# Optimization experiments

Hardware: AMD Instinct MI355X
Metric: run time of the kernel (lower is better)

The kernel has to match this reference:

```python
import jax, jax.numpy as jnp
import numpy as np

H = 1024          # hidden_size
E = 2 * H         # expansion e
S_DIM = 128       # shared q/k dim s
B, S = 4, 2048


def setup_inputs() -> dict:
    key = jax.random.key(0)
    ks = jax.random.split(key, 6)
    inputs = jax.random.normal(ks[0], (B, S, H), dtype=jnp.float32)
    W_uv = jax.random.normal(ks[1], (H, 2 * E + S_DIM), dtype=jnp.float32) * (1.0 / np.sqrt(H))
    b_uv = jnp.zeros((2 * E + S_DIM,), dtype=jnp.float32)
    gamma = jax.random.normal(ks[2], (2, S_DIM), dtype=jnp.float32) * 0.02
    beta = jnp.zeros((2, S_DIM), dtype=jnp.float32)
    W_out = jax.random.normal(ks[3], (E, H), dtype=jnp.float32) * (1.0 / np.sqrt(E))
    b_out = jnp.zeros((H,), dtype=jnp.float32)
    return {"inputs": inputs, "W_uv": W_uv, "b_uv": b_uv,
            "gamma": gamma, "beta": beta, "W_out": W_out, "b_out": b_out}


def reference(inputs, W_uv, b_uv, gamma, beta, W_out, b_out):
    seq_len = inputs.shape[1]
    # uv projection + SiLU
    uvb = jax.nn.silu(jnp.einsum('bsh,hf->bsf', inputs, W_uv) + b_uv)
    u = uvb[..., :E]                       # [B,S,E]
    v = uvb[..., E:2 * E]                  # [B,S,E]
    base = uvb[..., 2 * E:]                # [B,S,s]
    # per-head affine: [B,S,1,s]*[2,s] + [2,s] -> [B,S,2,s]
    qk = base[..., None, :] * gamma + beta
    q, k = qk[..., 0, :], qk[..., 1, :]    # [B,S,s] each
    scores = jnp.einsum('bns,bms->bnm', q, k) / seq_len   # [B,S,S]
    sq = jnp.square(jax.nn.relu(scores))
    attn_v = jnp.einsum('bnm,bme->bne', sq, v)            # [B,S,E]
    return jnp.einsum('bne,eh->bnh', u * attn_v, W_out) + b_out
```

## Files before the change

### kernel.cpp

```cpp
#include <hip/hip_runtime.h>
#include <stdint.h>


#define H_DIM  1024
#define E_DIM  2048
#define SD     128
#define B_SZ   4
#define S_LEN  2048
#define M_TOT  (B_SZ * S_LEN)
#define F_DIM  (2 * E_DIM + SD)

typedef _Float16 f16;
typedef __attribute__((ext_vector_type(4))) _Float16 f16x4;
typedef __attribute__((ext_vector_type(8))) _Float16 f16x8;
typedef __attribute__((ext_vector_type(4))) float f32x4;

__device__ __forceinline__ float silu_f(float x) { return x / (1.f + __expf(-x)); }

__device__ __forceinline__ void gload16(const void* g, void* l) {
  __builtin_amdgcn_global_load_lds(
      (const __attribute__((address_space(1))) void*)(uintptr_t)g,
      (__attribute__((address_space(3))) void*)(uint32_t)(uintptr_t)l,
      16, 0, 0);
}

__global__ __launch_bounds__(256) void cast_f16_k(const float* __restrict__ src,
                                                  f16* __restrict__ dst, long n) {
  long i = ((long)blockIdx.x * 256 + threadIdx.x) * 4;
  if (i < n) {
    float4 v = *(const float4*)(src + i);
    f16x4 h; h[0] = (f16)v.x; h[1] = (f16)v.y; h[2] = (f16)v.z; h[3] = (f16)v.w;
    *(f16x4*)(dst + i) = h;
  }
}

__global__ __launch_bounds__(256) void transpose_cast_k(const float* __restrict__ src,
                                                        f16* __restrict__ dst, int R, int C) {
  __shared__ float tile[32][33];
  int c0 = blockIdx.x * 32, r0 = blockIdx.y * 32;
  int tx = threadIdx.x & 31, ty = threadIdx.x >> 5;
  for (int i = ty; i < 32; i += 8) tile[i][tx] = src[(long)(r0 + i) * C + c0 + tx];
  __syncthreads();
  for (int i = ty; i < 32; i += 8) dst[(long)(c0 + i) * R + r0 + tx] = (f16)tile[tx][i];
}

template <int MODE>
__global__ __launch_bounds__(256) void mfma_gemm(
    const f16* __restrict__ Ag, const f16* __restrict__ Bg,
    float* __restrict__ F0, f16* __restrict__ H0, const f16* __restrict__ H1,
    f16* __restrict__ H2, f16* __restrict__ H3,
    const float* __restrict__ C0, const float* __restrict__ C1,
    const float* __restrict__ C2)
{
  constexpr int K   = (MODE == 1) ? SD : (MODE == 0 || MODE == 4) ? H_DIM : 2048;
  constexpr int LDA = K, LDB = K;

  __shared__ f16 As[128][32];
  __shared__ f16 Bs[128][32];

  const int t    = threadIdx.x;
  const int w    = t >> 6;
  const int lane = t & 63;
  const int l16  = lane & 15;
  const int quad = lane >> 4;
  const int wy   = w >> 1, wx = w & 1;
  const int m0   = blockIdx.y * 128;
  const int n0   = blockIdx.x * 128;
  const long z   = blockIdx.z;

  const f16* A = Ag + (MODE == 1 ? z * (long)S_LEN * SD
                     : MODE == 2 ? z * (long)S_LEN * S_LEN : 0);
  const f16* B = Bg + (MODE == 1 ? z * (long)S_LEN * SD
                     : MODE == 2 ? z * (long)E_DIM * S_LEN : 0);

  const int srow = lane >> 2;
  const int scol = (lane & 3) * 8;

  f32x4 acc[4][4] = {};

  for (int k0 = 0; k0 < K; k0 += 32) {
    const f16* gA = A + (long)(m0 + (w << 5) + srow) * LDA + k0 + scol;
    const f16* gB = B + (long)(n0 + (w << 5) + srow) * LDB + k0 + scol;
    gload16(gA,                  &As[(w << 5)][0]);
    gload16(gA + (long)16 * LDA, &As[(w << 5) + 16][0]);
    gload16(gB,                  &Bs[(w << 5)][0]);
    gload16(gB + (long)16 * LDB, &Bs[(w << 5) + 16][0]);
    __syncthreads();

    f16x8 av[4], bv[4];
#pragma unroll
    for (int i = 0; i < 4; i++)
      av[i] = *(const f16x8*)&As[(wy << 6) + (i << 4) + l16][quad << 3];
#pragma unroll
    for (int j = 0; j < 4; j++)
      bv[j] = *(const f16x8*)&Bs[(wx << 6) + (j << 4) + l16][quad << 3];
#pragma unroll
    for (int i = 0; i < 4; i++)
#pragma unroll
      for (int j = 0; j < 4; j++)
        acc[i][j] = __builtin_amdgcn_mfma_f32_16x16x32_f16(av[i], bv[j], acc[i][j], 0, 0, 0);
    __syncthreads();
  }

  const int rbase = m0 + (wy << 6) + (quad << 2);
  const int cbase = n0 + (wx << 6) + l16;

  if (MODE == 0) {
    if (n0 < E_DIM) {
#pragma unroll
      for (int i = 0; i < 4; i++)
#pragma unroll
        for (int j = 0; j < 4; j++) {
          int gc = cbase + (j << 4);
          float bias = C0[gc];
#pragma unroll
          for (int r = 0; r < 4; r++) {
            int gr = rbase + (i << 4) + r;
            H0[(long)gr * E_DIM + gc] = (f16)silu_f(acc[i][j][r] + bias);
          }
        }
    } else {
#pragma unroll
      for (int i = 0; i < 4; i++) {
        int gr0 = rbase + (i << 4);
        int b   = gr0 >> 11;
        int s0  = gr0 & (S_LEN - 1);
#pragma unroll
        for (int j = 0; j < 4; j++) {
          int gc = cbase + (j << 4);
          float bias = C0[gc];
          f16x4 pk;
#pragma unroll
          for (int r = 0; r < 4; r++) pk[r] = (f16)silu_f(acc[i][j][r] + bias);
          *(f16x4*)&H1[((long)b * E_DIM + (gc - E_DIM)) * S_LEN + s0] = pk;
        }
      }
    }
  } else if (MODE == 4) {
#pragma unroll
    for (int i = 0; i < 4; i++)
#pragma unroll
      for (int j = 0; j < 4; j++) {
        int jj = cbase + (j << 4);
        float bias = C0[jj];
        float g0 = C1[jj], g1 = C1[SD + jj];
        float be0 = C2[jj], be1 = C2[SD + jj];
#pragma unroll
        for (int r = 0; r < 4; r++) {
          int gr = rbase + (i << 4) + r;
          float s = silu_f(acc[i][j][r] + bias);
          H2[(long)gr * SD + jj] = (f16)(s * g0 + be0);
          H3[(long)gr * SD + jj] = (f16)(s * g1 + be1);
        }
      }
  } else if (MODE == 1) {
#pragma unroll
    for (int i = 0; i < 4; i++)
#pragma unroll
      for (int j = 0; j < 4; j++) {
        int gc = cbase + (j << 4);
#pragma unroll
        for (int r = 0; r < 4; r++) {
          int gr = rbase + (i << 4) + r;
          float tv = fmaxf(acc[i][j][r], 0.f) * 64.f;
          H0[z * (long)S_LEN * S_LEN + (long)gr * S_LEN + gc] = (f16)(tv * tv);
        }
      }
  } else if (MODE == 2) {
    const long rowoff = z * S_LEN;
#pragma unroll
    for (int i = 0; i < 4; i++)
#pragma unroll
      for (int j = 0; j < 4; j++) {
        int gc = cbase + (j << 4);
#pragma unroll
        for (int r = 0; r < 4; r++) {
          int gr = rbase + (i << 4) + r;
          long idx = (rowoff + gr) * (long)E_DIM + gc;
          H0[idx] = (f16)((float)H1[idx] * acc[i][j][r]);
        }
      }
  } else {
#pragma unroll
    for (int i = 0; i < 4; i++)
#pragma unroll
      for (int j = 0; j < 4; j++) {
        int gc = cbase + (j << 4);
        float bias = C0[gc];
#pragma unroll
        for (int r = 0; r < 4; r++) {
          int gr = rbase + (i << 4) + r;
          F0[(long)gr * H_DIM + gc] = acc[i][j][r] * (1.0f / 17179869184.0f) + bias;
        }
      }
  }
}

extern "C" void kernel_launch(void* const* d_in, const int* in_sizes, int n_in,
                              void* d_out, int out_size, void* d_ws, size_t ws_size,
                              hipStream_t stream) {
  const float* X     = (const float*)d_in[0];
  const float* W_uv  = (const float*)d_in[1];
  const float* b_uv  = (const float*)d_in[2];
  const float* gamma = (const float*)d_in[3];
  const float* beta  = (const float*)d_in[4];
  const float* W_out = (const float*)d_in[5];
  const float* b_out = (const float*)d_in[6];
  float* out = (float*)d_out;

  char* wp = (char*)d_ws;
  f16* Xh   = (f16*)wp; wp += (long)M_TOT * H_DIM * 2;
  f16* Wuvt = (f16*)wp; wp += (long)F_DIM * H_DIM * 2;
  f16* Wt   = (f16*)wp; wp += (long)H_DIM * E_DIM * 2;
  f16* u    = (f16*)wp; wp += (long)M_TOT * E_DIM * 2;
  f16* vt   = (f16*)wp; wp += (long)M_TOT * E_DIM * 2;
  f16* qh   = (f16*)wp; wp += (long)M_TOT * SD * 2;
  f16* kh   = (f16*)wp; wp += (long)M_TOT * SD * 2;
  f16* sq   = (f16*)wp; wp += (long)B_SZ * S_LEN * S_LEN * 2;
  f16* p    = (f16*)wp; wp += (long)M_TOT * E_DIM * 2;

  cast_f16_k<<<(M_TOT * H_DIM) / (256 * 4), 256, 0, stream>>>(X, Xh, (long)M_TOT * H_DIM);
  transpose_cast_k<<<dim3(F_DIM / 32, H_DIM / 32), 256, 0, stream>>>(W_uv, Wuvt, H_DIM, F_DIM);
  transpose_cast_k<<<dim3(H_DIM / 32, E_DIM / 32), 256, 0, stream>>>(W_out, Wt, E_DIM, H_DIM);

  mfma_gemm<0><<<dim3(2 * E_DIM / 128, M_TOT / 128, 1), 256, 0, stream>>>(
      Xh, Wuvt, nullptr, u, vt, nullptr, nullptr, b_uv, nullptr, nullptr);

  mfma_gemm<4><<<dim3(1, M_TOT / 128, 1), 256, 0, stream>>>(
      Xh, Wuvt + (long)2 * E_DIM * H_DIM, nullptr, nullptr, nullptr, qh, kh,
      b_uv + 2 * E_DIM, gamma, beta);

  mfma_gemm<1><<<dim3(S_LEN / 128, S_LEN / 128, B_SZ), 256, 0, stream>>>(
      qh, kh, nullptr, sq, nullptr, nullptr, nullptr, nullptr, nullptr, nullptr);

  mfma_gemm<2><<<dim3(E_DIM / 128, S_LEN / 128, B_SZ), 256, 0, stream>>>(
      sq, vt, nullptr, p, u, nullptr, nullptr, nullptr, nullptr, nullptr);

  mfma_gemm<3><<<dim3(H_DIM / 128, M_TOT / 128, 1), 256, 0, stream>>>(
      p, Wt, out, nullptr, nullptr, nullptr, nullptr, b_out, nullptr, nullptr);
}
```

Measured before the change: 404.7 us.

## Switch GEMM core to 32x32x16 MFMA with 64-wide K steps

Each wave now uses 2x2 tiles of the 32x32x16 f16 MFMA instead of 4x4 tiles of 16x16x32, and every K iteration loads 64 elements into two LDS halves. This halves the number of barrier pairs and cuts LDS fragment reads per MFMA, aiming for higher matrix-core throughput. Epilogue index math is rewritten for the 32x32 output layout. LDS use doubles, and there is still no overlap between loads and compute, and possible LDS bank conflicts.

Result: no change. 411.2 us (+1.6%).

```diff
diff --git a/kernel.cpp b/kernel.cpp
--- a/kernel.cpp
+++ b/kernel.cpp
@@ -13,7 +13,7 @@
 typedef _Float16 f16;
 typedef __attribute__((ext_vector_type(4))) _Float16 f16x4;
 typedef __attribute__((ext_vector_type(8))) _Float16 f16x8;
-typedef __attribute__((ext_vector_type(4))) float f32x4;
+typedef __attribute__((ext_vector_type(16))) float f32x16;
 
 __device__ __forceinline__ float silu_f(float x) { return x / (1.f + __expf(-x)); }
 
@@ -55,14 +55,14 @@
   constexpr int K   = (MODE == 1) ? SD : (MODE == 0 || MODE == 4) ? H_DIM : 2048;
   constexpr int LDA = K, LDB = K;
 
-  __shared__ f16 As[128][32];
-  __shared__ f16 Bs[128][32];
+  __shared__ f16 As[2][128][32];
+  __shared__ f16 Bs[2][128][32];
 
   const int t    = threadIdx.x;
   const int w    = t >> 6;
   const int lane = t & 63;
-  const int l16  = lane & 15;
-  const int quad = lane >> 4;
+  const int lo5  = lane & 31;
+  const int hi   = lane >> 5;
   const int wy   = w >> 1, wx = w & 1;
   const int m0   = blockIdx.y * 128;
   const int n0   = blockIdx.x * 128;
@@ -76,122 +76,142 @@
   const int srow = lane >> 2;
   const int scol = (lane & 3) * 8;
 
-  f32x4 acc[4][4] = {};
-
-  for (int k0 = 0; k0 < K; k0 += 32) {
-    const f16* gA = A + (long)(m0 + (w << 5) + srow) * LDA + k0 + scol;
-    const f16* gB = B + (long)(n0 + (w << 5) + srow) * LDB + k0 + scol;
-    gload16(gA,                  &As[(w << 5)][0]);
-    gload16(gA + (long)16 * LDA, &As[(w << 5) + 16][0]);
-    gload16(gB,                  &Bs[(w << 5)][0]);
-    gload16(gB + (long)16 * LDB, &Bs[(w << 5) + 16][0]);
+  f32x16 acc[2][2] = {};
+
+  for (int k0 = 0; k0 < K; k0 += 64) {
+#pragma unroll
+    for (int h = 0; h < 2; h++)
+#pragma unroll
+      for (int g16 = 0; g16 < 2; g16++) {
+        const int r = (w << 5) + (g16 << 4);
+        gload16(A + (long)(m0 + r + srow) * LDA + k0 + (h << 5) + scol, &As[h][r][0]);
+        gload16(B + (long)(n0 + r + srow) * LDB + k0 + (h << 5) + scol, &Bs[h][r][0]);
+      }
     __syncthreads();
 
-    f16x8 av[4], bv[4];
-#pragma unroll
-    for (int i = 0; i < 4; i++)
-      av[i] = *(const f16x8*)&As[(wy << 6) + (i << 4) + l16][quad << 3];
-#pragma unroll
-    for (int j = 0; j < 4; j++)
-      bv[j] = *(const f16x8*)&Bs[(wx << 6) + (j << 4) + l16][quad << 3];
-#pragma unroll
-    for (int i = 0; i < 4; i++)
-#pragma unroll
-      for (int j = 0; j < 4; j++)
-        acc[i][j] = __builtin_amdgcn_mfma_f32_16x16x32_f16(av[i], bv[j], acc[i][j], 0, 0, 0);
+#pragma unroll
+    for (int ks = 0; ks < 4; ks++) {
+      const int h  = ks >> 1;
+      const int kc = (ks & 1) * 16 + (hi << 3);
+      f16x8 av[2], bv[2];
+#pragma unroll
+      for (int i = 0; i < 2; i++)
+        av[i] = *(const f16x8*)&As[h][(wy << 6) + (i << 5) + lo5][kc];
+#pragma unroll
+      for (int j = 0; j < 2; j++)
+        bv[j] = *(const f16x8*)&Bs[h][(wx << 6) + (j << 5) + lo5][kc];
+#pragma unroll
+      for (int i = 0; i < 2; i++)
+#pragma unroll
+        for (int j = 0; j < 2; j++)
+          acc[i][j] = __builtin_amdgcn_mfma_f32_32x32x16_f16(av[i], bv[j], acc[i][j], 0, 0, 0);
+    }
     __syncthreads();
   }
 
-  const int rbase = m0 + (wy << 6) + (quad << 2);
-  const int cbase = n0 + (wx << 6) + l16;
+  const int rb0 = m0 + (wy << 6) + (hi << 2);
+  const int cb0 = n0 + (wx << 6) + lo5;
 
   if (MODE == 0) {
     if (n0 < E_DIM) {
 #pragma unroll
-      for (int i = 0; i < 4; i++)
-#pragma unroll
-        for (int j = 0; j < 4; j++) {
-          int gc = cbase + (j << 4);
+      for (int i = 0; i < 2; i++)
+#pragma unroll
+        for (int j = 0; j < 2; j++) {
+          int gc = cb0 + (j << 5);
           float bias = C0[gc];
 #pragma unroll
-          for (int r = 0; r < 4; r++) {
-            int gr = rbase + (i << 4) + r;
-            H0[(long)gr * E_DIM + gc] = (f16)silu_f(acc[i][j][r] + bias);
-          }
+          for (int g = 0; g < 4; g++)
+#pragma unroll
+            for (int rr = 0; rr < 4; rr++) {
+              int gr = rb0 + (i << 5) + (g << 3) + rr;
+              H0[(long)gr * E_DIM + gc] = (f16)silu_f(acc[i][j][g * 4 + rr] + bias);
+            }
         }
     } else {
 #pragma unroll
-      for (int i = 0; i < 4; i++) {
-        int gr0 = rbase + (i << 4);
-        int b   = gr0 >> 11;
-        int s0  = gr0 & (S_LEN - 1);
-#pragma unroll
-        for (int j = 0; j < 4; j++) {
-          int gc = cbase + (j << 4);
+      for (int i = 0; i < 2; i++) {
+#pragma unroll
+        for (int j = 0; j < 2; j++) {
+          int gc = cb0 + (j << 5);
           float bias = C0[gc];
-          f16x4 pk;
-#pragma unroll
-          for (int r = 0; r < 4; r++) pk[r] = (f16)silu_f(acc[i][j][r] + bias);
-          *(f16x4*)&H1[((long)b * E_DIM + (gc - E_DIM)) * S_LEN + s0] = pk;
+#pragma unroll
+          for (int g = 0; g < 4; g++) {
+            int gr0 = rb0 + (i << 5) + (g << 3);
+            int b   = gr0 >> 11;
+            int s0  = gr0 & (S_LEN - 1);
+            f16x4 pk;
+#pragma unroll
+            for (int rr = 0; rr < 4; rr++) pk[rr] = (f16)silu_f(acc[i][j][g * 4 + rr] + bias);
+            *(f16x4*)&H1[((long)b * E_DIM + (gc - E_DIM)) * S_LEN + s0] = pk;
+          }
         }
       }
     }
   } else if (MODE == 4) {
 #pragma unroll
-    for (int i = 0; i < 4; i++)
-#pragma unroll
-      for (int j = 0; j < 4; j++) {
-        int jj = cbase + (j << 4);
+    for (int i = 0; i < 2; i++)
+#pragma unroll
+      for (int j = 0; j < 2; j++) {
+        int jj = cb0 + (j << 5);
         float bias = C0[jj];
         float g0 = C1[jj], g1 = C1[SD + jj];
         float be0 = C2[jj], be1 = C2[SD + jj];
 #pragma unroll
-        for (int r = 0; r < 4; r++) {
-          int gr = rbase + (i << 4) + r;
-          float s = silu_f(acc[i][j][r] + bias);
-          H2[(long)gr * SD + jj] = (f16)(s * g0 + be0);
-          H3[(long)gr * SD + jj] = (f16)(s * g1 + be1);
-        }
+        for (int g = 0; g < 4; g++)
+#pragma unroll
+          for (int rr = 0; rr < 4; rr++) {
+            int gr = rb0 + (i << 5) + (g << 3) + rr;
+            float s = silu_f(acc[i][j][g * 4 + rr] + bias);
+            H2[(long)gr * SD + jj] = (f16)(s * g0 + be0);
+            H3[(long)gr * SD + jj] = (f16)(s * g1 + be1);
+          }
       }
   } else if (MODE == 1) {
 #pragma unroll
-    for (int i = 0; i < 4; i++)
-#pragma unroll
-      for (int j = 0; j < 4; j++) {
-        int gc = cbase + (j << 4);
-#pragma unroll
-        for (int r = 0; r < 4; r++) {
-          int gr = rbase + (i << 4) + r;
-          float tv = fmaxf(acc[i][j][r], 0.f) * 64.f;
-          H0[z * (long)S_LEN * S_LEN + (long)gr * S_LEN + gc] = (f16)(tv * tv);
-        }
+    for (int i = 0; i < 2; i++)
+#pragma unroll
+      for (int j = 0; j < 2; j++) {
+        int gc = cb0 + (j << 5);
+#pragma unroll
+        for (int g = 0; g < 4; g++)
+#pragma unroll
+          for (int rr = 0; rr < 4; rr++) {
+            int gr = rb0 + (i << 5) + (g << 3) + rr;
+            float tv = fmaxf(acc[i][j][g * 4 + rr], 0.f) * 64.f;
+            H0[z * (long)S_LEN * S_LEN + (long)gr * S_LEN + gc] = (f16)(tv * tv);
+          }
       }
   } else if (MODE == 2) {
     const long rowoff = z * S_LEN;
 #pragma unroll
-    for (int i = 0; i < 4; i++)
-#pragma unroll
-      for (int j = 0; j < 4; j++) {
-        int gc = cbase + (j << 4);
-#pragma unroll
-        for (int r = 0; r < 4; r++) {
-          int gr = rbase + (i << 4) + r;
-          long idx = (rowoff + gr) * (long)E_DIM + gc;
-          H0[idx] = (f16)((float)H1[idx] * acc[i][j][r]);
-        }
+    for (int i = 0; i < 2; i++)
+#pragma unroll
+      for (int j = 0; j < 2; j++) {
+        int gc = cb0 + (j << 5);
+#pragma unroll
+        for (int g = 0; g < 4; g++)
+#pragma unroll
+          for (int rr = 0; rr < 4; rr++) {
+            int gr = rb0 + (i << 5) + (g << 3) + rr;
+            long idx = (rowoff + gr) * (long)E_DIM + gc;
+            H0[idx] = (f16)((float)H1[idx] * acc[i][j][g * 4 + rr]);
+          }
       }
   } else {
 #pragma unroll
-    for (int i = 0; i < 4; i++)
-#pragma unroll
-      for (int j = 0; j < 4; j++) {
-        int gc = cbase + (j << 4);
+    for (int i = 0; i < 2; i++)
+#pragma unroll
+      for (int j = 0; j < 2; j++) {
+        int gc = cb0 + (j << 5);
         float bias = C0[gc];
 #pragma unroll
-        for (int r = 0; r < 4; r++) {
-          int gr = rbase + (i << 4) + r;
-          F0[(long)gr * H_DIM + gc] = acc[i][j][r] * (1.0f / 17179869184.0f) + bias;
-        }
+        for (int g = 0; g < 4; g++)
+#pragma unroll
+          for (int rr = 0; rr < 4; rr++) {
+            int gr = rb0 + (i << 5) + (g << 3) + rr;
+            F0[(long)gr * H_DIM + gc] = acc[i][j][g * 4 + rr] * (1.0f / 17179869184.0f) + bias;
+          }
       }
   }
 }
```
